# Kernel tuning notes

Measured on AMD Instinct MI355X. Metric: run time of the kernel, lower is better.

Reference implementation:

```python
import jax, jax.numpy as jnp
import numpy as np

MAX_LEN = 16


def setup_inputs() -> dict:
    key = jax.random.key(0)
    ks = jax.random.split(key, 12)
    B, F, H, E, V = 4096, 512, 256, 128, 32000
    s = lambda k, shp, scale: jax.random.normal(k, shp, dtype=jnp.float32) * scale
    return {
        "x": s(ks[0], (B, F), 1.0),
        "W_in": s(ks[1], (H, F), 1.0 / np.sqrt(F)),
        "b_in": jnp.zeros((H,), jnp.float32),
        "W_out": s(ks[2], (V, H), 1.0 / np.sqrt(H)),
        "b_out": jnp.zeros((V,), jnp.float32),
        "emb": s(ks[3], (V, E), 1.0),
        "sos": s(ks[4], (E,), 0.01),
        "W_ih": s(ks[5], (4 * H, E), 1.0 / np.sqrt(H)),
        "W_hh": s(ks[6], (4 * H, H), 1.0 / np.sqrt(H)),
        "b_ih": jnp.zeros((4 * H,), jnp.float32),
        "b_hh": jnp.zeros((4 * H,), jnp.float32),
    }


def reference(x, W_in, b_in, W_out, b_out, emb, sos, W_ih, W_hh, b_ih, b_hh):
    B = x.shape[0]
    H = W_in.shape[0]
    h0 = x @ W_in.T + b_in                      # embed_input -> initial hidden, [B,H]
    c0 = jnp.zeros_like(h0)
    inp0 = jnp.broadcast_to(sos, (B, sos.shape[0]))  # sos embedding, [B,E]
    keys = jax.random.split(jax.random.key(42), MAX_LEN)

    def step(carry, key):
        h, c, inp = carry
        gates = inp @ W_ih.T + b_ih + h @ W_hh.T + b_hh   # [B,4H]
        i, f, g, o = jnp.split(gates, 4, axis=1)          # torch LSTMCell gate order
        i, f, o = jax.nn.sigmoid(i), jax.nn.sigmoid(f), jax.nn.sigmoid(o)
        g = jnp.tanh(g)
        c = f * c + i * g
        h = o * jnp.tanh(c)
        logp = jax.nn.log_softmax(h @ W_out.T + b_out, axis=1)  # [B,V]
        sample = jax.random.categorical(key, logp, axis=1)      # [B] int
        lp = jnp.take_along_axis(logp, sample[:, None], axis=1)[:, 0]
        ent = -jnp.sum(jnp.exp(logp) * logp, axis=1)
        new_inp = emb[sample]                                   # embedding lookup
        return (h, c, new_inp), (sample, lp, ent)

    _, (seq, lps, ents) = jax.lax.scan(step, (h0, c0, inp0), keys)
    seq = seq.T           # [B, max_len]
    lps = lps.T
    ents = ents.T
    zf = jnp.zeros((B, 1), jnp.float32)
    sequence = jnp.concatenate([seq, jnp.zeros((B, 1), seq.dtype)], axis=1)
    logits = jnp.concatenate([lps, zf], axis=1)
    entropy = jnp.concatenate([ents, zf], axis=1)
    return sequence, logits, entropy
```

## Files before the change

kernel.cpp:

```cpp
#include <hip/hip_runtime.h>
#include <stdint.h>

#define B   4096
#define F   512
#define H   256
#define E   128
#define V   32000
#define TT  16
#define OC  17
#define NCH 6
#define NTILES 250
#define NSLOT (NCH * 4)
#define RSCALE 2048.0f
#define RINV   4.8828125e-4f

typedef _Float16 half8 __attribute__((ext_vector_type(8)));
typedef float f32x4 __attribute__((ext_vector_type(4)));
typedef unsigned short us8 __attribute__((ext_vector_type(8)));

__host__ __device__ __forceinline__ uint32_t tf_rotl(uint32_t x, int r) {
    return (x << r) | (x >> (32 - r));
}

#define TF_R(rot) { x0 += x1; x1 = tf_rotl(x1, rot); x1 ^= x0; }

__host__ __device__ __forceinline__ void tf2x32(uint32_t k0, uint32_t k1,
                                                uint32_t c0, uint32_t c1,
                                                uint32_t& o0, uint32_t& o1) {
    uint32_t k2 = k0 ^ k1 ^ 0x1BD11BDAu;
    uint32_t x0 = c0 + k0, x1 = c1 + k1;
    TF_R(13) TF_R(15) TF_R(26) TF_R(6)
    x0 += k1; x1 += k2 + 1u;
    TF_R(17) TF_R(29) TF_R(16) TF_R(24)
    x0 += k2; x1 += k0 + 2u;
    TF_R(13) TF_R(15) TF_R(26) TF_R(6)
    x0 += k0; x1 += k1 + 3u;
    TF_R(17) TF_R(29) TF_R(16) TF_R(24)
    x0 += k1; x1 += k2 + 4u;
    TF_R(13) TF_R(15) TF_R(26) TF_R(6)
    x0 += k2; x1 += k0 + 5u;
    o0 = x0; o1 = x1;
}

__device__ __forceinline__ void split2h(float x, unsigned short& u1, unsigned short& u2) {
    _Float16 a = (_Float16)x;
    float r = (x - (float)a) * RSCALE;
    _Float16 b = (_Float16)r;
    u1 = __builtin_bit_cast(unsigned short, a);
    u2 = __builtin_bit_cast(unsigned short, b);
}

__global__ void k_init(float* __restrict__ c, float* __restrict__ inp,
                       const float* __restrict__ sos, float* __restrict__ out) {
    int i = blockIdx.x * 256 + threadIdx.x;
    if (i < B * H) c[i] = 0.f;
    if (i < B * E) inp[i] = sos[i & (E - 1)];
    if (i < 3 * B) {
        int o = i >> 12, r = i & (B - 1);
        out[(size_t)o * (B * OC) + (size_t)r * OC + (OC - 1)] = 0.f;
    }
}

__global__ __launch_bounds__(256) void k_wsplit(const float* __restrict__ W,
                                                unsigned short* __restrict__ w1,
                                                unsigned short* __restrict__ w2) {
    int i = blockIdx.x * 256 + threadIdx.x;
    float4 v = *(const float4*)(W + (size_t)i * 4);
    ushort4 p1, p2;
    split2h(v.x, p1.x, p2.x);
    split2h(v.y, p1.y, p2.y);
    split2h(v.z, p1.z, p2.z);
    split2h(v.w, p1.w, p2.w);
    *(ushort4*)(w1 + (size_t)i * 4) = p1;
    *(ushort4*)(w2 + (size_t)i * 4) = p2;
}

__global__ __launch_bounds__(256) void k_h0(const float* __restrict__ x,
                                            const float* __restrict__ W_in,
                                            const float* __restrict__ b_in,
                                            float* __restrict__ h) {
    __shared__ float xs[16 * 512];
    __shared__ float wt[16 * 260];
    const int tid = threadIdx.x;
    const int r0 = blockIdx.x * 16;

#pragma unroll
    for (int p = 0; p < 8; p++) {
        int ff = tid + 256 * p, row = ff >> 7, c4 = ff & 127;
        *(float4*)&xs[row * 512 + c4 * 4] =
            *(const float4*)(x + (size_t)(r0 + row) * 512 + c4 * 4);
    }
    const int g = tid >> 6, l = tid & 63;
    float acc[4][4] = {{0.f}};

    for (int kc = 0; kc < 32; kc++) {
        __syncthreads();
#pragma unroll
        for (int p = 0; p < 4; p++) {
            int ff = tid + 256 * p, rl = ff >> 2, k4 = ff & 3;
            float4 w = *(const float4*)(W_in + (size_t)rl * 512 + kc * 16 + k4 * 4);
            wt[(k4 * 4 + 0) * 260 + rl] = w.x;
            wt[(k4 * 4 + 1) * 260 + rl] = w.y;
            wt[(k4 * 4 + 2) * 260 + rl] = w.z;
            wt[(k4 * 4 + 3) * 260 + rl] = w.w;
        }
        __syncthreads();
#pragma unroll
        for (int kk = 0; kk < 16; kk += 4) {
            float4 w0 = *(const float4*)&wt[(kk + 0) * 260 + 4 * l];
            float4 w1 = *(const float4*)&wt[(kk + 1) * 260 + 4 * l];
            float4 w2 = *(const float4*)&wt[(kk + 2) * 260 + 4 * l];
            float4 w3 = *(const float4*)&wt[(kk + 3) * 260 + 4 * l];
#pragma unroll
            for (int b = 0; b < 4; b++) {
                float4 xb = *(const float4*)&xs[(4 * g + b) * 512 + kc * 16 + kk];
                acc[b][0] = fmaf(xb.w, w3.x, fmaf(xb.z, w2.x, fmaf(xb.y, w1.x, fmaf(xb.x, w0.x, acc[b][0]))));
                acc[b][1] = fmaf(xb.w, w3.y, fmaf(xb.z, w2.y, fmaf(xb.y, w1.y, fmaf(xb.x, w0.y, acc[b][1]))));
                acc[b][2] = fmaf(xb.w, w3.z, fmaf(xb.z, w2.z, fmaf(xb.y, w1.z, fmaf(xb.x, w0.z, acc[b][2]))));
                acc[b][3] = fmaf(xb.w, w3.w, fmaf(xb.z, w2.w, fmaf(xb.y, w1.w, fmaf(xb.x, w0.w, acc[b][3]))));
            }
        }
    }
    float4 bi = *(const float4*)(b_in + 4 * l);
#pragma unroll
    for (int b = 0; b < 4; b++) {
        float4 o = make_float4(acc[b][0] + bi.x, acc[b][1] + bi.y,
                               acc[b][2] + bi.z, acc[b][3] + bi.w);
        *(float4*)(h + (size_t)(r0 + 4 * g + b) * 256 + 4 * l) = o;
    }
}

__global__ __launch_bounds__(256) void k_gates_lstm(
    const float* __restrict__ inp, const float* __restrict__ hcur,
    const float* __restrict__ W_ih, const float* __restrict__ W_hh,
    const float* __restrict__ b_ih, const float* __restrict__ b_hh,
    float* __restrict__ c, float* __restrict__ hnxt,
    unsigned short* __restrict__ hsp1, unsigned short* __restrict__ hsp2) {
    __shared__ float xs[16 * 384];
    __shared__ float wt[32 * 260];
    const int tid = threadIdx.x;
    const int r0 = blockIdx.x * 16;
    const int u0 = blockIdx.y * 64;

#pragma unroll
    for (int p = 0; p < 2; p++) {
        int ff = tid + 256 * p, row = ff >> 5, c4 = ff & 31;
        *(float4*)&xs[row * 384 + c4 * 4] =
            *(const float4*)(inp + (size_t)(r0 + row) * 128 + c4 * 4);
    }
#pragma unroll
    for (int p = 0; p < 4; p++) {
        int ff = tid + 256 * p, row = ff >> 6, c4 = ff & 63;
        *(float4*)&xs[row * 384 + 128 + c4 * 4] =
            *(const float4*)(hcur + (size_t)(r0 + row) * 256 + c4 * 4);
    }
    const int g = tid >> 6, l = tid & 63;
    float acc[4][4] = {{0.f}};

    for (int kc = 0; kc < 12; kc++) {
        __syncthreads();
        {
            const float* src; int rowlen, koff;
            if (kc < 4) { src = W_ih; rowlen = 128; koff = kc * 32; }
            else        { src = W_hh; rowlen = 256; koff = (kc - 4) * 32; }
#pragma unroll
            for (int p = 0; p < 8; p++) {
                int rl = (tid >> 3) + 32 * p;
                int k4 = tid & 7;
                int grow = ((rl >> 6) << 8) + u0 + (rl & 63);
                float4 w = *(const float4*)(src + (size_t)grow * rowlen + koff + k4 * 4);
                wt[(k4 * 4 + 0) * 260 + rl] = w.x;
                wt[(k4 * 4 + 1) * 260 + rl] = w.y;
                wt[(k4 * 4 + 2) * 260 + rl] = w.z;
                wt[(k4 * 4 + 3) * 260 + rl] = w.w;
            }
        }
        __syncthreads();
#pragma unroll
        for (int kk = 0; kk < 32; kk += 4) {
            float4 w0 = *(const float4*)&wt[(kk + 0) * 260 + 4 * l];
            float4 w1 = *(const float4*)&wt[(kk + 1) * 260 + 4 * l];
            float4 w2 = *(const float4*)&wt[(kk + 2) * 260 + 4 * l];
            float4 w3 = *(const float4*)&wt[(kk + 3) * 260 + 4 * l];
#pragma unroll
            for (int b = 0; b < 4; b++) {
                float4 xb = *(const float4*)&xs[(4 * g + b) * 384 + kc * 32 + kk];
                acc[b][0] = fmaf(xb.w, w3.x, fmaf(xb.z, w2.x, fmaf(xb.y, w1.x, fmaf(xb.x, w0.x, acc[b][0]))));
                acc[b][1] = fmaf(xb.w, w3.y, fmaf(xb.z, w2.y, fmaf(xb.y, w1.y, fmaf(xb.x, w0.y, acc[b][1]))));
                acc[b][2] = fmaf(xb.w, w3.z, fmaf(xb.z, w2.z, fmaf(xb.y, w1.z, fmaf(xb.x, w0.z, acc[b][2]))));
                acc[b][3] = fmaf(xb.w, w3.w, fmaf(xb.z, w2.w, fmaf(xb.y, w1.w, fmaf(xb.x, w0.w, acc[b][3]))));
            }
        }
    }
    {
        int rl0 = 4 * l;
        int grow0 = ((rl0 >> 6) << 8) + u0 + (rl0 & 63);
        float4 bi = *(const float4*)(b_ih + grow0);
        float4 bh = *(const float4*)(b_hh + grow0);
#pragma unroll
        for (int b = 0; b < 4; b++) {
            acc[b][0] += bi.x + bh.x; acc[b][1] += bi.y + bh.y;
            acc[b][2] += bi.z + bh.z; acc[b][3] += bi.w + bh.w;
        }
    }
    __syncthreads();
    float* gl = wt;
#pragma unroll
    for (int b = 0; b < 4; b++)
        *(float4*)&gl[(4 * g + b) * 256 + 4 * l] =
            make_float4(acc[b][0], acc[b][1], acc[b][2], acc[b][3]);
    __syncthreads();
    {
        int bl = tid >> 4, uq = tid & 15;
        size_t cidx = (size_t)(r0 + bl) * 256 + u0 + uq * 4;
        float4 cold4 = *(float4*)(c + cidx);
        float4 cv, hv;
#pragma unroll
        for (int j = 0; j < 4; j++) {
            int ul = uq * 4 + j;
            float gi = gl[bl * 256 + ul];
            float gf = gl[bl * 256 + 64 + ul];
            float gg = gl[bl * 256 + 128 + ul];
            float go = gl[bl * 256 + 192 + ul];
            float si = fmaf(0.5f, tanhf(0.5f * gi), 0.5f);
            float sf = fmaf(0.5f, tanhf(0.5f * gf), 0.5f);
            float so = fmaf(0.5f, tanhf(0.5f * go), 0.5f);
            float tg = tanhf(gg);
            float cold = (&cold4.x)[j];
            float cn = sf * cold + si * tg;
            (&cv.x)[j] = cn;
            (&hv.x)[j] = so * tanhf(cn);
        }
        *(float4*)(c + cidx) = cv;
        *(float4*)(hnxt + cidx) = hv;
        ushort4 p1, p2;
        split2h(hv.x, p1.x, p2.x);
        split2h(hv.y, p1.y, p2.y);
        split2h(hv.z, p1.z, p2.z);
        split2h(hv.w, p1.w, p2.w);
        *(ushort4*)(hsp1 + cidx) = p1;
        *(ushort4*)(hsp2 + cidx) = p2;
    }
}

__global__ __launch_bounds__(256, 3) void k_logits_sample(
    const unsigned short* __restrict__ hsp1, const unsigned short* __restrict__ hsp2,
    const unsigned short* __restrict__ wb1, const unsigned short* __restrict__ wb2,
    const float* __restrict__ b_out, unsigned key0, unsigned key1,
    float* __restrict__ part) {
    __shared__ unsigned short As[16384];
    const int tid = threadIdx.x;
    const int w = tid >> 6, lane = tid & 63;
    const int quad = lane >> 4, n4 = lane & 15;
    const int r0 = blockIdx.x * 32;
    const int chunk = blockIdx.y;

#pragma unroll
    for (int p = 0; p < 8; p++) {
        int idx8 = tid + 256 * p;
        int f = idx8 >> 6, lo = idx8 & 63;
        int kc = f >> 2, s = (f >> 1) & 1, mt = f & 1;
        const unsigned short* hs = s ? hsp2 : hsp1;
        us8 v = *(const us8*)(hs + (size_t)(r0 + mt * 16 + (lo & 15)) * 256
                                 + kc * 32 + (lo >> 4) * 8);
        *(us8*)&As[f * 512 + lo * 8] = v;
    }
    __syncthreads();

    float S[8], Ts[8], U[8], La[8]; int Ai[8];
#pragma unroll
    for (int b = 0; b < 8; b++) { S[b] = 0.f; Ts[b] = 0.f; U[b] = -3.4e38f; La[b] = 0.f; Ai[b] = 0; }

    for (int tile = chunk; tile < NTILES; tile += NCH) {
        const int v0 = tile * 128;
        const int nbase = v0 + w * 32 + n4;
        f32x4 ah[2][2], al[2][2];
#pragma unroll
        for (int mt = 0; mt < 2; mt++)
#pragma unroll
            for (int nt = 0; nt < 2; nt++) {
                ah[mt][nt] = (f32x4){0.f, 0.f, 0.f, 0.f};
                al[mt][nt] = (f32x4){0.f, 0.f, 0.f, 0.f};
            }

#pragma unroll
        for (int kc = 0; kc < 8; kc++) {
            half8 a[2][2];
#pragma unroll
            for (int s = 0; s < 2; s++)
#pragma unroll
                for (int mt = 0; mt < 2; mt++)
                    a[s][mt] = *(const half8*)&As[(((kc * 2 + s) * 2 + mt)) * 512 + lane * 8];
#pragma unroll
            for (int nt = 0; nt < 2; nt++) {
                size_t boff = (size_t)(nbase + nt * 16) * 256 + kc * 32 + quad * 8;
                half8 b1 = *(const half8*)(wb1 + boff);
                half8 b2 = *(const half8*)(wb2 + boff);
#pragma unroll
                for (int mt = 0; mt < 2; mt++) {
                    ah[mt][nt] = __builtin_amdgcn_mfma_f32_16x16x32_f16(a[0][mt], b1, ah[mt][nt], 0, 0, 0);
                    al[mt][nt] = __builtin_amdgcn_mfma_f32_16x16x32_f16(a[0][mt], b2, al[mt][nt], 0, 0, 0);
                    al[mt][nt] = __builtin_amdgcn_mfma_f32_16x16x32_f16(a[1][mt], b1, al[mt][nt], 0, 0, 0);
                }
            }
        }
#pragma unroll
        for (int nt = 0; nt < 2; nt++) {
            const int v = nbase + nt * 16;
            float bo = b_out[v];
#pragma unroll
            for (int mt = 0; mt < 2; mt++) {
#pragma unroll
                for (int j = 0; j < 4; j++) {
                    float lg = fmaf(RINV, al[mt][nt][j], ah[mt][nt][j]) + bo;
                    float e = __expf(lg - 20.f);
                    int si = mt * 4 + j;
                    S[si] += e;
                    Ts[si] = fmaf(e, lg, Ts[si]);
                    unsigned row = (unsigned)(r0 + mt * 16 + quad * 4 + j);
                    unsigned o0, o1;
                    tf2x32(key0, key1, 0u, row * (unsigned)V + (unsigned)v, o0, o1);
                    unsigned bits = o0 ^ o1;
                    float f = __uint_as_float((bits >> 9) | 0x3f800000u) - 1.0f;
                    float uu = fmaxf(1.17549435e-38f, f + 1.17549435e-38f);
                    float gmb = -logf(-logf(uu));
                    float u = lg + gmb;
                    if (u > U[si] || (u == U[si] && v < Ai[si])) { U[si] = u; Ai[si] = v; La[si] = lg; }
                }
            }
        }
    }
#pragma unroll
    for (int si = 0; si < 8; si++) {
        float s = S[si], ts = Ts[si], u = U[si], la = La[si]; int a = Ai[si];
#pragma unroll
        for (int off = 1; off < 16; off <<= 1) {
            s  += __shfl_xor(s, off);
            ts += __shfl_xor(ts, off);
            float u2 = __shfl_xor(u, off);
            float la2 = __shfl_xor(la, off);
            int a2 = __shfl_xor(a, off);
            if (u2 > u || (u2 == u && a2 < a)) { u = u2; a = a2; la = la2; }
        }
        if (n4 == 0) {
            int mt = si >> 2, reg = si & 3;
            int row = r0 + mt * 16 + quad * 4 + reg;
            float* p = part + (size_t)row * NSLOT * 8 + (chunk * 4 + w) * 8;
            p[0] = s; p[1] = ts; p[2] = u; p[3] = la;
            ((int*)p)[4] = a;
        }
    }
}

__global__ __launch_bounds__(256) void k_sample_out(
    const float* __restrict__ part, const float* __restrict__ emb,
    float* __restrict__ inp, float* __restrict__ out, int step) {
    const int tid = threadIdx.x;
    const int row = blockIdx.x * 8 + (tid >> 5);
    const int lane = tid & 31;
    const float* p = part + (size_t)row * NSLOT * 8;
    float s = 0.f, ts = 0.f, u = -3.4e38f, la = 0.f; int a = 0;
    for (int cg = 0; cg < NSLOT; cg++) {
        const float* q = p + cg * 8;
        s += q[0]; ts += q[1];
        float uc = q[2]; int ac = ((const int*)q)[4];
        if (uc > u || (uc == u && ac < a)) { u = uc; a = ac; la = q[3]; }
    }
    float lse = logf(s) + 20.f;
    if (lane == 0) {
        out[(size_t)row * OC + step] = (float)a;
        out[(size_t)B * OC + (size_t)row * OC + step] = la - lse;
        out[(size_t)2 * B * OC + (size_t)row * OC + step] = lse - ts / s;
    }
    float4 e4 = *(const float4*)(emb + (size_t)a * 128 + lane * 4);
    *(float4*)&inp[(size_t)row * 128 + lane * 4] = e4;
}

extern "C" void kernel_launch(void* const* d_in, const int* in_sizes, int n_in,
                              void* d_out, int out_size, void* d_ws, size_t ws_size,
                              hipStream_t stream) {
    (void)in_sizes; (void)n_in; (void)out_size; (void)ws_size;
    const float* x     = (const float*)d_in[0];
    const float* W_in  = (const float*)d_in[1];
    const float* b_in  = (const float*)d_in[2];
    const float* W_out = (const float*)d_in[3];
    const float* b_out = (const float*)d_in[4];
    const float* emb   = (const float*)d_in[5];
    const float* sos   = (const float*)d_in[6];
    const float* W_ih  = (const float*)d_in[7];
    const float* W_hh  = (const float*)d_in[8];
    const float* b_ih  = (const float*)d_in[9];
    const float* b_hh  = (const float*)d_in[10];
    float* out = (float*)d_out;
    float* ws  = (float*)d_ws;

    float* hA   = ws;
    float* hB   = ws + 1048576;
    float* cc   = ws + 2097152;
    float* inp  = ws + 3145728;
    float* part = ws + 3670016;
    unsigned short* hsp1 = (unsigned short*)(ws + 4456448);
    unsigned short* hsp2 = (unsigned short*)(ws + 4980736);
    unsigned short* wb1  = (unsigned short*)(ws + 5505024);
    unsigned short* wb2  = (unsigned short*)(ws + 9601024);

    unsigned K0[TT], K1[TT];
    for (int t = 0; t < TT; t++) {
        uint32_t o0, o1;
        tf2x32(0u, 42u, 0u, (uint32_t)t, o0, o1);
        K0[t] = o0; K1[t] = o1;
    }

    k_init<<<4096, 256, 0, stream>>>(cc, inp, sos, out);
    k_wsplit<<<V * H / 4 / 256, 256, 0, stream>>>(W_out, wb1, wb2);
    k_h0<<<B / 16, 256, 0, stream>>>(x, W_in, b_in, hA);

    float* hc = hA;
    float* hn = hB;
    for (int t = 0; t < TT; t++) {
        k_gates_lstm<<<dim3(B / 16, 4), 256, 0, stream>>>(inp, hc, W_ih, W_hh,
                                                          b_ih, b_hh, cc, hn, hsp1, hsp2);
        k_logits_sample<<<dim3(B / 32, NCH), 256, 0, stream>>>(hsp1, hsp2, wb1, wb2,
                                                               b_out, K0[t], K1[t], part);
        k_sample_out<<<B / 8, 256, 0, stream>>>(part, emb, inp, out, t);
        float* tmp = hc; hc = hn; hn = tmp;
    }
}
```

Measured before the change: 13.71 ms.

## Keep W_out tile in registers and stream hidden rows in logits kernel

The logits/sampling kernel now holds a 64-column slice of W_out resident in registers as split fp16 hi/lo pairs, converted on the fly from fp32, and loops over 1024 batch rows. The A operand (hidden state) is streamed from global memory instead of being staged in LDS. The separate weight-split kernel and its workspace buffers are removed. Partial reductions are combined across waves through LDS and written per tile, 500 partials per row, and k_sample_out reduces them with warp shuffles. The aim is to avoid rereading the weight matrix for each row block. The trade-offs are much larger partial traffic, a per-row-group __syncthreads and per-element shuffle reductions, and high register pressure.

```diff
diff --git a/kernel.cpp b/kernel.cpp
--- a/kernel.cpp
+++ b/kernel.cpp
@@ -8,9 +8,10 @@
 #define V   32000
 #define TT  16
 #define OC  17
-#define NCH 6
-#define NTILES 250
-#define NSLOT (NCH * 4)
+#define NT64 500
+#define RQ   4
+#define PSTR 6
+#define PROWSTR (NT64 * PSTR)
 #define RSCALE 2048.0f
 #define RINV   4.8828125e-4f
 
@@ -61,20 +62,6 @@
     }
 }
 
-__global__ __launch_bounds__(256) void k_wsplit(const float* __restrict__ W,
-                                                unsigned short* __restrict__ w1,
-                                                unsigned short* __restrict__ w2) {
-    int i = blockIdx.x * 256 + threadIdx.x;
-    float4 v = *(const float4*)(W + (size_t)i * 4);
-    ushort4 p1, p2;
-    split2h(v.x, p1.x, p2.x);
-    split2h(v.y, p1.y, p2.y);
-    split2h(v.z, p1.z, p2.z);
-    split2h(v.w, p1.w, p2.w);
-    *(ushort4*)(w1 + (size_t)i * 4) = p1;
-    *(ushort4*)(w2 + (size_t)i * 4) = p2;
-}
-
 __global__ __launch_bounds__(256) void k_h0(const float* __restrict__ x,
                                             const float* __restrict__ W_in,
                                             const float* __restrict__ b_in,
@@ -245,110 +232,111 @@
 
 __global__ __launch_bounds__(256, 3) void k_logits_sample(
     const unsigned short* __restrict__ hsp1, const unsigned short* __restrict__ hsp2,
-    const unsigned short* __restrict__ wb1, const unsigned short* __restrict__ wb2,
-    const float* __restrict__ b_out, unsigned key0, unsigned key1,
-    float* __restrict__ part) {
-    __shared__ unsigned short As[16384];
+    const float* __restrict__ W_out, const float* __restrict__ b_out,
+    unsigned key0, unsigned key1, float* __restrict__ part) {
+    __shared__ float red[4][32][5];
     const int tid = threadIdx.x;
     const int w = tid >> 6, lane = tid & 63;
     const int quad = lane >> 4, n4 = lane & 15;
-    const int r0 = blockIdx.x * 32;
-    const int chunk = blockIdx.y;
-
-#pragma unroll
-    for (int p = 0; p < 8; p++) {
-        int idx8 = tid + 256 * p;
-        int f = idx8 >> 6, lo = idx8 & 63;
-        int kc = f >> 2, s = (f >> 1) & 1, mt = f & 1;
-        const unsigned short* hs = s ? hsp2 : hsp1;
-        us8 v = *(const us8*)(hs + (size_t)(r0 + mt * 16 + (lo & 15)) * 256
-                                 + kc * 32 + (lo >> 4) * 8);
-        *(us8*)&As[f * 512 + lo * 8] = v;
-    }
-    __syncthreads();
-
-    float S[8], Ts[8], U[8], La[8]; int Ai[8];
-#pragma unroll
-    for (int b = 0; b < 8; b++) { S[b] = 0.f; Ts[b] = 0.f; U[b] = -3.4e38f; La[b] = 0.f; Ai[b] = 0; }
-
-    for (int tile = chunk; tile < NTILES; tile += NCH) {
-        const int v0 = tile * 128;
-        const int nbase = v0 + w * 32 + n4;
-        f32x4 ah[2][2], al[2][2];
-#pragma unroll
-        for (int mt = 0; mt < 2; mt++)
-#pragma unroll
-            for (int nt = 0; nt < 2; nt++) {
-                ah[mt][nt] = (f32x4){0.f, 0.f, 0.f, 0.f};
-                al[mt][nt] = (f32x4){0.f, 0.f, 0.f, 0.f};
-            }
-
+    const int tile = blockIdx.x % NT64;
+    const int q    = blockIdx.x / NT64;
+    const int v    = tile * 64 + w * 16 + n4;
+
+    half8 b1[8], b2[8];
+#pragma unroll
+    for (int kc = 0; kc < 8; kc++) {
+        const float* wp = W_out + (size_t)v * 256 + kc * 32 + quad * 8;
+        float4 wa = *(const float4*)wp;
+        float4 wb = *(const float4*)(wp + 4);
+        float wv[8] = {wa.x, wa.y, wa.z, wa.w, wb.x, wb.y, wb.z, wb.w};
+#pragma unroll
+        for (int j = 0; j < 8; j++) {
+            _Float16 hi = (_Float16)wv[j];
+            float r = (wv[j] - (float)hi) * RSCALE;
+            b1[kc][j] = hi;
+            b2[kc][j] = (_Float16)r;
+        }
+    }
+    const float bo = b_out[v];
+
+#pragma unroll 1
+    for (int rg = 0; rg < 32; rg++) {
+        const int r0 = q * 1024 + rg * 32;
+        f32x4 ah[2], al[2];
+#pragma unroll
+        for (int mt = 0; mt < 2; mt++) {
+            ah[mt] = (f32x4){0.f, 0.f, 0.f, 0.f};
+            al[mt] = (f32x4){0.f, 0.f, 0.f, 0.f};
+        }
 #pragma unroll
         for (int kc = 0; kc < 8; kc++) {
-            half8 a[2][2];
-#pragma unroll
-            for (int s = 0; s < 2; s++)
-#pragma unroll
-                for (int mt = 0; mt < 2; mt++)
-                    a[s][mt] = *(const half8*)&As[(((kc * 2 + s) * 2 + mt)) * 512 + lane * 8];
-#pragma unroll
-            for (int nt = 0; nt < 2; nt++) {
-                size_t boff = (size_t)(nbase + nt * 16) * 256 + kc * 32 + quad * 8;
-                half8 b1 = *(const half8*)(wb1 + boff);
-                half8 b2 = *(const half8*)(wb2 + boff);
-#pragma unroll
-                for (int mt = 0; mt < 2; mt++) {
-                    ah[mt][nt] = __builtin_amdgcn_mfma_f32_16x16x32_f16(a[0][mt], b1, ah[mt][nt], 0, 0, 0);
-                    al[mt][nt] = __builtin_amdgcn_mfma_f32_16x16x32_f16(a[0][mt], b2, al[mt][nt], 0, 0, 0);
-                    al[mt][nt] = __builtin_amdgcn_mfma_f32_16x16x32_f16(a[1][mt], b1, al[mt][nt], 0, 0, 0);
+            size_t abase = (size_t)(r0 + n4) * 256 + kc * 32 + quad * 8;
+            half8 a1m0 = *(const half8*)(hsp1 + abase);
+            half8 a1m1 = *(const half8*)(hsp1 + abase + 16 * 256);
+            half8 a2m0 = *(const half8*)(hsp2 + abase);
+            half8 a2m1 = *(const half8*)(hsp2 + abase + 16 * 256);
+            ah[0] = __builtin_amdgcn_mfma_f32_16x16x32_f16(a1m0, b1[kc], ah[0], 0, 0, 0);
+            al[0] = __builtin_amdgcn_mfma_f32_16x16x32_f16(a1m0, b2[kc], al[0], 0, 0, 0);
+            al[0] = __builtin_amdgcn_mfma_f32_16x16x32_f16(a2m0, b1[kc], al[0], 0, 0, 0);
+            ah[1] = __builtin_amdgcn_mfma_f32_16x16x32_f16(a1m1, b1[kc], ah[1], 0, 0, 0);
+            al[1] = __builtin_amdgcn_mfma_f32_16x16x32_f16(a1m1, b2[kc], al[1], 0, 0, 0);
+            al[1] = __builtin_amdgcn_mfma_f32_16x16x32_f16(a2m1, b1[kc], al[1], 0, 0, 0);
+        }
+#pragma unroll
+        for (int mt = 0; mt < 2; mt++) {
+#pragma unroll
+            for (int j = 0; j < 4; j++) {
+                float lg = fmaf(RINV, al[mt][j], ah[mt][j]) + bo;
+                float e = __expf(lg - 20.f);
+                float ts = fmaf(e, lg, 0.f);
+                unsigned row = (unsigned)(r0 + mt * 16 + quad * 4 + j);
+                unsigned o0, o1;
+                tf2x32(key0, key1, 0u, row * (unsigned)V + (unsigned)v, o0, o1);
+                unsigned bits = o0 ^ o1;
+                float f = __uint_as_float((bits >> 9) | 0x3f800000u) - 1.0f;
+                float uu = fmaxf(1.17549435e-38f, f + 1.17549435e-38f);
+                float gmb = -logf(-logf(uu));
+                float ut = lg + gmb;
+                float s = e, la = lg; int ai = v;
+#pragma unroll
+                for (int off = 1; off < 16; off <<= 1) {
+                    s  += __shfl_xor(s, off);
+                    ts += __shfl_xor(ts, off);
+                    float u2 = __shfl_xor(ut, off);
+                    float la2 = __shfl_xor(la, off);
+                    int a2 = __shfl_xor(ai, off);
+                    if (u2 > ut || (u2 == ut && a2 < ai)) { ut = u2; ai = a2; la = la2; }
+                }
+                if (n4 == 0) {
+                    int rl = mt * 16 + quad * 4 + j;
+                    red[w][rl][0] = s;
+                    red[w][rl][1] = ts;
+                    red[w][rl][2] = ut;
+                    red[w][rl][3] = la;
+                    ((int*)red[w][rl])[4] = ai;
                 }
             }
         }
-#pragma unroll
-        for (int nt = 0; nt < 2; nt++) {
-            const int v = nbase + nt * 16;
-            float bo = b_out[v];
-#pragma unroll
-            for (int mt = 0; mt < 2; mt++) {
-#pragma unroll
-                for (int j = 0; j < 4; j++) {
-                    float lg = fmaf(RINV, al[mt][nt][j], ah[mt][nt][j]) + bo;
-                    float e = __expf(lg - 20.f);
-                    int si = mt * 4 + j;
-                    S[si] += e;
-                    Ts[si] = fmaf(e, lg, Ts[si]);
-                    unsigned row = (unsigned)(r0 + mt * 16 + quad * 4 + j);
-                    unsigned o0, o1;
-                    tf2x32(key0, key1, 0u, row * (unsigned)V + (unsigned)v, o0, o1);
-                    unsigned bits = o0 ^ o1;
-                    float f = __uint_as_float((bits >> 9) | 0x3f800000u) - 1.0f;
-                    float uu = fmaxf(1.17549435e-38f, f + 1.17549435e-38f);
-                    float gmb = -logf(-logf(uu));
-                    float u = lg + gmb;
-                    if (u > U[si] || (u == U[si] && v < Ai[si])) { U[si] = u; Ai[si] = v; La[si] = lg; }
+        __syncthreads();
+        if (tid < 32) {
+            float s = red[0][tid][0] + red[1][tid][0] + red[2][tid][0] + red[3][tid][0];
+            float ts = red[0][tid][1] + red[1][tid][1] + red[2][tid][1] + red[3][tid][1];
+            float ut = red[0][tid][2];
+            float la = red[0][tid][3];
+            int ai = ((int*)red[0][tid])[4];
+#pragma unroll
+            for (int w2 = 1; w2 < 4; w2++) {
+                float u2 = red[w2][tid][2];
+                int a2 = ((int*)red[w2][tid])[4];
+                if (u2 > ut || (u2 == ut && a2 < ai)) {
+                    ut = u2; ai = a2; la = red[w2][tid][3];
                 }
             }
-        }
-    }
-#pragma unroll
-    for (int si = 0; si < 8; si++) {
-        float s = S[si], ts = Ts[si], u = U[si], la = La[si]; int a = Ai[si];
-#pragma unroll
-        for (int off = 1; off < 16; off <<= 1) {
-            s  += __shfl_xor(s, off);
-            ts += __shfl_xor(ts, off);
-            float u2 = __shfl_xor(u, off);
-            float la2 = __shfl_xor(la, off);
-            int a2 = __shfl_xor(a, off);
-            if (u2 > u || (u2 == u && a2 < a)) { u = u2; a = a2; la = la2; }
-        }
-        if (n4 == 0) {
-            int mt = si >> 2, reg = si & 3;
-            int row = r0 + mt * 16 + quad * 4 + reg;
-            float* p = part + (size_t)row * NSLOT * 8 + (chunk * 4 + w) * 8;
-            p[0] = s; p[1] = ts; p[2] = u; p[3] = la;
-            ((int*)p)[4] = a;
-        }
+            float* p = part + (size_t)(r0 + tid) * PROWSTR + tile * PSTR;
+            p[0] = s; p[1] = ts; p[2] = ut; p[3] = la;
+            ((int*)p)[4] = ai;
+        }
+        __syncthreads();
     }
 }
 
@@ -358,13 +346,22 @@
     const int tid = threadIdx.x;
     const int row = blockIdx.x * 8 + (tid >> 5);
     const int lane = tid & 31;
-    const float* p = part + (size_t)row * NSLOT * 8;
-    float s = 0.f, ts = 0.f, u = -3.4e38f, la = 0.f; int a = 0;
-    for (int cg = 0; cg < NSLOT; cg++) {
-        const float* q = p + cg * 8;
-        s += q[0]; ts += q[1];
-        float uc = q[2]; int ac = ((const int*)q)[4];
-        if (uc > u || (uc == u && ac < a)) { u = uc; a = ac; la = q[3]; }
+    const float* p = part + (size_t)row * PROWSTR;
+    float s = 0.f, ts = 0.f, ut = -3.4e38f, la = 0.f; int a = 0;
+    for (int cg = lane; cg < NT64; cg += 32) {
+        const float* qq = p + cg * PSTR;
+        s += qq[0]; ts += qq[1];
+        float uc = qq[2]; int ac = ((const int*)qq)[4];
+        if (uc > ut || (uc == ut && ac < a)) { ut = uc; a = ac; la = qq[3]; }
+    }
+#pragma unroll
+    for (int off = 1; off < 32; off <<= 1) {
+        s  += __shfl_xor(s, off);
+        ts += __shfl_xor(ts, off);
+        float u2 = __shfl_xor(ut, off);
+        float la2 = __shfl_xor(la, off);
+        int a2 = __shfl_xor(a, off);
+        if (u2 > ut || (u2 == ut && a2 < a)) { ut = u2; a = a2; la = la2; }
     }
     float lse = logf(s) + 20.f;
     if (lane == 0) {
@@ -399,10 +396,8 @@
     float* cc   = ws + 2097152;
     float* inp  = ws + 3145728;
     float* part = ws + 3670016;
-    unsigned short* hsp1 = (unsigned short*)(ws + 4456448);
-    unsigned short* hsp2 = (unsigned short*)(ws + 4980736);
-    unsigned short* wb1  = (unsigned short*)(ws + 5505024);
-    unsigned short* wb2  = (unsigned short*)(ws + 9601024);
+    unsigned short* hsp1 = (unsigned short*)(ws + 15958016);
+    unsigned short* hsp2 = (unsigned short*)(ws + 16482304);
 
     unsigned K0[TT], K1[TT];
     for (int t = 0; t < TT; t++) {
@@ -412,7 +407,6 @@
     }
 
     k_init<<<4096, 256, 0, stream>>>(cc, inp, sos, out);
-    k_wsplit<<<V * H / 4 / 256, 256, 0, stream>>>(W_out, wb1, wb2);
     k_h0<<<B / 16, 256, 0, stream>>>(x, W_in, b_in, hA);
 
     float* hc = hA;
@@ -420,8 +414,8 @@
     for (int t = 0; t < TT; t++) {
         k_gates_lstm<<<dim3(B / 16, 4), 256, 0, stream>>>(inp, hc, W_ih, W_hh,
                                                           b_ih, b_hh, cc, hn, hsp1, hsp2);
-        k_logits_sample<<<dim3(B / 32, NCH), 256, 0, stream>>>(hsp1, hsp2, wb1, wb2,
-                                                               b_out, K0[t], K1[t], part);
+        k_logits_sample<<<NT64 * RQ, 256, 0, stream>>>(hsp1, hsp2, W_out, b_out,
+                                                       K0[t], K1[t], part);
         k_sample_out<<<B / 8, 256, 0, stream>>>(part, emb, inp, out, t);
         float* tmp = hc; hc = hn; hn = tmp;
     }
```

Measured after the change: 19.82 ms. 44.5% more time.
